# Optimization experiments

Measured on AMD Instinct MI355X. Metric: run time of the kernel, lower is better.

The kernel has to match this reference:

```python
import jax, jax.numpy as jnp
import numpy as np

B, H, W, K = 4, 512, 512, 8
BKG_DEPTH = 100.0  # sentinel depth for empty pixels, as in the torch module


def setup_inputs() -> dict:
    key = jax.random.key(0)
    k1, k2, k3 = jax.random.split(key, 3)
    pixel_colors = jax.random.uniform(k1, (B, H, W, K, 4), dtype=jnp.float32)
    zbuf = jax.random.normal(k2, (B, H, W, K), dtype=jnp.float32)  # <0 => invalid fragment
    pixel_labels = jax.random.randint(k3, (B, H, W, K), 0, K, dtype=jnp.int32)
    background_color = jnp.ones((3,), jnp.float32)
    return {
        "pixel_colors": pixel_colors,
        "zbuf": zbuf,
        "pixel_labels": pixel_labels,
        "background_color": background_color,
    }


def _composite(pixel_colors, zbuf, labels_f, background_color):
    """Back-to-front alpha-over compositing scan across the K layer axis."""
    Bq, Hq, Wq, Kd, _ = pixel_colors.shape
    # layer axis to front, reversed so scan runs k = K-1 .. 0 (back to front)
    cols = jnp.moveaxis(pixel_colors, 3, 0)[::-1]  # [K,B,H,W,4]
    deps = jnp.moveaxis(zbuf, 3, 0)[::-1]          # [K,B,H,W]
    labs = jnp.moveaxis(labels_f, 3, 0)[::-1]      # [K,B,H,W]

    rgb0 = jnp.broadcast_to(background_color.astype(pixel_colors.dtype), (Bq, Hq, Wq, 3)) + 0.0
    a0 = jnp.zeros((Bq, Hq, Wq), pixel_colors.dtype)
    d0 = jnp.full((Bq, Hq, Wq), BKG_DEPTH, pixel_colors.dtype)
    l0 = jnp.full((Bq, Hq, Wq), float(Kd), pixel_colors.dtype)

    def step(carry, x):
        rgb, a, d, lab = carry
        c, z, l = x
        alpha = c[..., 3]
        rgb = c[..., :3] * alpha[..., None] + rgb * (1.0 - alpha[..., None])
        a = jnp.maximum(alpha, a)
        d = jnp.where(z > 0, z * alpha + d * (1.0 - alpha), d)
        lab = jnp.where(jnp.isfinite(l), jnp.where(alpha > 0.5, l, lab), lab)
        return (rgb, a, d, lab), None

    (rgb, a, d, lab), _ = jax.lax.scan(step, (rgb0, a0, d0, l0), (cols, deps, labs))
    img = jnp.concatenate([rgb, a[..., None]], axis=-1)  # [B,H,W,4]
    return img, d, lab


def _human_images(pixel_colors, labels_int, background_color):
    """For each label n in [0,K): gather the first (front-most) fragment with that label."""
    Bq, Hq, Wq, Kd, C = pixel_colors.shape
    N = Kd
    hit = labels_int[..., None] == jnp.arange(N, dtype=labels_int.dtype)  # [B,H,W,K,N]
    hit = jnp.concatenate([hit, jnp.ones((Bq, Hq, Wq, 1, N), bool)], axis=3)  # void layer always hits
    first = jnp.argmax(hit, axis=3)  # [B,H,W,N], first k where label matches, else K
    pcv = jnp.concatenate(
        [pixel_colors, jnp.zeros((Bq, Hq, Wq, 1, C), pixel_colors.dtype)], axis=3
    )  # [B,H,W,K+1,4]
    gathered = jnp.take_along_axis(pcv, first[..., None], axis=3)  # [B,H,W,N,4]
    alpha = gathered[..., 3:4]
    rgb = gathered[..., :3] * alpha + background_color * (1.0 - alpha)
    return jnp.concatenate([rgb, alpha], axis=-1)  # [B,H,W,N,4]


def reference(pixel_colors, zbuf, pixel_labels, background_color):
    Kd = pixel_colors.shape[3]
    # labels as float with NaN marking invalid fragments (zbuf < 0), as in torch forward
    labels_f = jnp.where(zbuf < 0, jnp.nan, pixel_labels.astype(pixel_colors.dtype))
    composite_image, composite_depth, lab = _composite(pixel_colors, zbuf, labels_f, background_color)
    # labels as ints with -1 marking invalid, as in raster_each_labeled_human
    labels_int = jnp.where(zbuf < 0, -1, pixel_labels.astype(jnp.int32))
    human_images = _human_images(pixel_colors, labels_int, background_color)
    lab = jnp.where(lab > Kd - 0.5, -1.0, lab)
    composite_label = jnp.round(lab).astype(jnp.int32)
    return composite_image, composite_depth, composite_label, human_images
```

## Files before the change

### kernel.cpp

```cpp
#include <hip/hip_runtime.h>


#define BKG_DEPTH 100.0f
#define KD 8

__global__ __launch_bounds__(256) void alpha_comp_pixel(
    const float4* __restrict__ pc,
    const float4* __restrict__ zb4,
    const int4*   __restrict__ lb4,
    const float*  __restrict__ bg,
    float* __restrict__ out,
    int P)
{
    const int p = blockIdx.x * blockDim.x + threadIdx.x;
    if (p >= P) return;

    const float bg0 = bg[0], bg1 = bg[1], bg2 = bg[2];

    float4 c[KD];
    #pragma unroll
    for (int k = 0; k < KD; ++k) c[k] = pc[p * KD + k];

    const float4 zlo = zb4[p * 2 + 0];
    const float4 zhi = zb4[p * 2 + 1];
    const float z[KD] = {zlo.x, zlo.y, zlo.z, zlo.w, zhi.x, zhi.y, zhi.z, zhi.w};

    const int4 llo = lb4[p * 2 + 0];
    const int4 lhi = lb4[p * 2 + 1];
    const int l[KD] = {llo.x, llo.y, llo.z, llo.w, lhi.x, lhi.y, lhi.z, lhi.w};

    float T = 1.0f, r = 0.0f, g = 0.0f, b = 0.0f, am = 0.0f;
    #pragma unroll
    for (int k = 0; k < KD; ++k) {
        const float a = c[k].w;
        const float w = a * T;
        r = fmaf(c[k].x, w, r);
        g = fmaf(c[k].y, w, g);
        b = fmaf(c[k].z, w, b);
        am = fmaxf(am, a);
        T *= (1.0f - a);
    }
    r = fmaf(bg0, T, r);
    g = fmaf(bg1, T, g);
    b = fmaf(bg2, T, b);

    float T2 = 1.0f, d = 0.0f;
    #pragma unroll
    for (int k = 0; k < KD; ++k) {
        const float a2 = (z[k] > 0.0f) ? c[k].w : 0.0f;
        d = fmaf(z[k] * a2, T2, d);
        T2 *= (1.0f - a2);
    }
    d = fmaf(BKG_DEPTH, T2, d);

    float labv = -1.0f;
    #pragma unroll
    for (int k = KD - 1; k >= 0; --k) {
        const bool cond = (!(z[k] < 0.0f)) && (c[k].w > 0.5f);
        labv = cond ? (float)l[k] : labv;
    }

    ((float4*)out)[p] = make_float4(r, g, b, am);
    out[(size_t)4 * P + p] = d;
    out[(size_t)5 * P + p] = labv;

    float4* __restrict__ hout = (float4*)(out + (size_t)6 * P);
    #pragma unroll
    for (int n = 0; n < KD; ++n) {
        float gx = 0.0f, gy = 0.0f, gz = 0.0f, gw = 0.0f;
        #pragma unroll
        for (int k = KD - 1; k >= 0; --k) {
            const bool m = (!(z[k] < 0.0f)) && (l[k] == n);
            gx = m ? c[k].x : gx;
            gy = m ? c[k].y : gy;
            gz = m ? c[k].z : gz;
            gw = m ? c[k].w : gw;
        }
        const float ia = 1.0f - gw;
        hout[p * KD + n] = make_float4(fmaf(gx, gw, bg0 * ia),
                                       fmaf(gy, gw, bg1 * ia),
                                       fmaf(gz, gw, bg2 * ia),
                                       gw);
    }
}

extern "C" void kernel_launch(void* const* d_in, const int* in_sizes, int n_in,
                              void* d_out, int out_size, void* d_ws, size_t ws_size,
                              hipStream_t stream) {
    const float4* pc  = (const float4*)d_in[0];
    const float4* zb4 = (const float4*)d_in[1];
    const int4*   lb4 = (const int4*)d_in[2];
    const float*  bg  = (const float*)d_in[3];
    float* out = (float*)d_out;

    const int P = in_sizes[1] / KD;
    const int block = 256;
    const int grid = (P + block - 1) / block;
    alpha_comp_pixel<<<grid, block, 0, stream>>>(pc, zb4, lb4, bg, out, P);
}
```

Baseline: 326.4 us.

## Stage pixel colors and human-image outputs through swizzled LDS for coalesced access

```diff
diff --git a/kernel.cpp b/kernel.cpp
--- a/kernel.cpp
+++ b/kernel.cpp
@@ -3,8 +3,11 @@
 
 #define BKG_DEPTH 100.0f
 #define KD 8
+#define BLK 256
 
-__global__ __launch_bounds__(256) void alpha_comp_pixel(
+typedef float f32x4 __attribute__((ext_vector_type(4)));
+
+__global__ __launch_bounds__(256) void alpha_comp_lds(
     const float4* __restrict__ pc,
     const float4* __restrict__ zb4,
     const int4*   __restrict__ lb4,
@@ -12,22 +15,47 @@
     float* __restrict__ out,
     int P)
 {
-    const int p = blockIdx.x * blockDim.x + threadIdx.x;
-    if (p >= P) return;
+    __shared__ float4 cbuf[BLK * KD];
+
+    const int t    = threadIdx.x;
+    const int base = blockIdx.x * BLK;
+    const int p    = base + t;
+    const int pcl  = (p < P) ? p : (P - 1);
 
     const float bg0 = bg[0], bg1 = bg[1], bg2 = bg[2];
 
+    const float4 zlo = zb4[(size_t)pcl * 2 + 0];
+    const float4 zhi = zb4[(size_t)pcl * 2 + 1];
+    const int4   llo = lb4[(size_t)pcl * 2 + 0];
+    const int4   lhi = lb4[(size_t)pcl * 2 + 1];
+
+    {
+        const size_t fb = (size_t)base * KD;
+        const size_t fmax = (size_t)P * KD - 1;
+        float4 stg[8];
+        #pragma unroll
+        for (int i = 0; i < 8; ++i) {
+            size_t g = fb + i * BLK + t;
+            stg[i] = pc[g <= fmax ? g : fmax];
+        }
+        #pragma unroll
+        for (int i = 0; i < 8; ++i) {
+            const int g  = i * BLK + t;
+            const int pl = g >> 3;
+            const int k  = g & 7;
+            cbuf[pl * KD + (k ^ (pl & 7))] = stg[i];
+        }
+    }
+    __syncthreads();
+
     float4 c[KD];
     #pragma unroll
-    for (int k = 0; k < KD; ++k) c[k] = pc[p * KD + k];
+    for (int k = 0; k < KD; ++k)
+        c[k] = cbuf[t * KD + (k ^ (t & 7))];
+    __syncthreads();
 
-    const float4 zlo = zb4[p * 2 + 0];
-    const float4 zhi = zb4[p * 2 + 1];
     const float z[KD] = {zlo.x, zlo.y, zlo.z, zlo.w, zhi.x, zhi.y, zhi.z, zhi.w};
-
-    const int4 llo = lb4[p * 2 + 0];
-    const int4 lhi = lb4[p * 2 + 1];
-    const int l[KD] = {llo.x, llo.y, llo.z, llo.w, lhi.x, lhi.y, lhi.z, lhi.w};
+    const int   l[KD] = {llo.x, llo.y, llo.z, llo.w, lhi.x, lhi.y, lhi.z, lhi.w};
 
     float T = 1.0f, r = 0.0f, g = 0.0f, b = 0.0f, am = 0.0f;
     #pragma unroll
@@ -60,11 +88,12 @@
         labv = cond ? (float)l[k] : labv;
     }
 
-    ((float4*)out)[p] = make_float4(r, g, b, am);
-    out[(size_t)4 * P + p] = d;
-    out[(size_t)5 * P + p] = labv;
+    if (p < P) {
+        ((float4*)out)[p] = make_float4(r, g, b, am);
+        out[(size_t)4 * P + p] = d;
+        out[(size_t)5 * P + p] = labv;
+    }
 
-    float4* __restrict__ hout = (float4*)(out + (size_t)6 * P);
     #pragma unroll
     for (int n = 0; n < KD; ++n) {
         float gx = 0.0f, gy = 0.0f, gz = 0.0f, gw = 0.0f;
@@ -77,10 +106,28 @@
             gw = m ? c[k].w : gw;
         }
         const float ia = 1.0f - gw;
-        hout[p * KD + n] = make_float4(fmaf(gx, gw, bg0 * ia),
-                                       fmaf(gy, gw, bg1 * ia),
-                                       fmaf(gz, gw, bg2 * ia),
-                                       gw);
+        cbuf[t * KD + (n ^ (t & 7))] = make_float4(fmaf(gx, gw, bg0 * ia),
+                                                   fmaf(gy, gw, bg1 * ia),
+                                                   fmaf(gz, gw, bg2 * ia),
+                                                   gw);
+    }
+    __syncthreads();
+
+    {
+        f32x4* __restrict__ hout = (f32x4*)(out + (size_t)6 * P);
+        const size_t fb = (size_t)base * KD;
+        #pragma unroll
+        for (int i = 0; i < 8; ++i) {
+            const int g  = i * BLK + t;
+            const int pl = g >> 3;
+            const int n  = g & 7;
+            const float4 v = cbuf[pl * KD + (n ^ (pl & 7))];
+            const size_t go = fb + g;
+            if (go < (size_t)P * KD) {
+                f32x4 vv = {v.x, v.y, v.z, v.w};
+                __builtin_nontemporal_store(vv, &hout[go]);
+            }
+        }
     }
 }
 
@@ -94,7 +141,7 @@
     float* out = (float*)d_out;
 
     const int P = in_sizes[1] / KD;
-    const int block = 256;
+    const int block = BLK;
     const int grid = (P + block - 1) / block;
-    alpha_comp_pixel<<<grid, block, 0, stream>>>(pc, zb4, lb4, bg, out, P);
+    alpha_comp_lds<<<grid, block, 0, stream>>>(pc, zb4, lb4, bg, out, P);
 }
```

Result: faster. 308.2 us (-5.6%).

## Split each pixel across eight lanes with DPP scans and coalesced I/O

Applied to the files above, without the earlier changes.

```diff
diff --git a/kernel.cpp b/kernel.cpp
--- a/kernel.cpp
+++ b/kernel.cpp
@@ -4,97 +4,127 @@
 #define BKG_DEPTH 100.0f
 #define KD 8
 
-__global__ __launch_bounds__(256) void alpha_comp_pixel(
+typedef float f32x4 __attribute__((ext_vector_type(4)));
+
+#define QP_XOR1 0xB1
+#define QP_XOR2 0x4E
+#define ROW_SHL(n) (0x100 | (n))
+#define ROW_SHR(n) (0x110 | (n))
+
+template <int CTRL>
+__device__ __forceinline__ float dppf(float x) {
+    return __int_as_float(__builtin_amdgcn_update_dpp(
+        0, __float_as_int(x), CTRL, 0xF, 0xF, true));
+}
+template <int CTRL>
+__device__ __forceinline__ int dppi(int x) {
+    return __builtin_amdgcn_update_dpp(0, x, CTRL, 0xF, 0xF, true);
+}
+
+__global__ __launch_bounds__(256) void alpha_comp_dpp(
     const float4* __restrict__ pc,
-    const float4* __restrict__ zb4,
-    const int4*   __restrict__ lb4,
+    const float*  __restrict__ zb,
+    const int*    __restrict__ lb,
     const float*  __restrict__ bg,
     float* __restrict__ out,
     int P)
 {
-    const int p = blockIdx.x * blockDim.x + threadIdx.x;
-    if (p >= P) return;
+    const int tid = blockIdx.x * blockDim.x + threadIdx.x;
+    const int pix = tid >> 3;
+    const int kk  = tid & 7;
+    if (pix >= P) return;
 
     const float bg0 = bg[0], bg1 = bg[1], bg2 = bg[2];
 
-    float4 c[KD];
-    #pragma unroll
-    for (int k = 0; k < KD; ++k) c[k] = pc[p * KD + k];
+    const float4 c     = pc[tid];
+    const float  z     = zb[tid];
+    const int    lbl   = lb[tid];
+    const float  alpha = c.w;
+    const bool   valid = !(z < 0.0f);
 
-    const float4 zlo = zb4[p * 2 + 0];
-    const float4 zhi = zb4[p * 2 + 1];
-    const float z[KD] = {zlo.x, zlo.y, zlo.z, zlo.w, zhi.x, zhi.y, zhi.z, zhi.w};
+    float incl = 1.0f - alpha;
+    { const float u = dppf<ROW_SHR(1)>(incl); incl = (kk >= 1) ? incl * u : incl; }
+    { const float u = dppf<ROW_SHR(2)>(incl); incl = (kk >= 2) ? incl * u : incl; }
+    { const float u = dppf<ROW_SHR(4)>(incl); incl = (kk >= 4) ? incl * u : incl; }
+    float pre = dppf<ROW_SHR(1)>(incl); pre = (kk == 0) ? 1.0f : pre;
+    const float T = dppf<ROW_SHL(7)>(incl);
+    const float w = alpha * pre;
 
-    const int4 llo = lb4[p * 2 + 0];
-    const int4 lhi = lb4[p * 2 + 1];
-    const int l[KD] = {llo.x, llo.y, llo.z, llo.w, lhi.x, lhi.y, lhi.z, lhi.w};
+    float sr = c.x * w, sg = c.y * w, sb = c.z * w, am = alpha;
+    sr += dppf<QP_XOR1>(sr); sg += dppf<QP_XOR1>(sg); sb += dppf<QP_XOR1>(sb);
+    am = fmaxf(am, dppf<QP_XOR1>(am));
+    sr += dppf<QP_XOR2>(sr); sg += dppf<QP_XOR2>(sg); sb += dppf<QP_XOR2>(sb);
+    am = fmaxf(am, dppf<QP_XOR2>(am));
+    sr += dppf<ROW_SHL(4)>(sr); sg += dppf<ROW_SHL(4)>(sg); sb += dppf<ROW_SHL(4)>(sb);
+    am = fmaxf(am, dppf<ROW_SHL(4)>(am));
 
-    float T = 1.0f, r = 0.0f, g = 0.0f, b = 0.0f, am = 0.0f;
-    #pragma unroll
-    for (int k = 0; k < KD; ++k) {
-        const float a = c[k].w;
-        const float w = a * T;
-        r = fmaf(c[k].x, w, r);
-        g = fmaf(c[k].y, w, g);
-        b = fmaf(c[k].z, w, b);
-        am = fmaxf(am, a);
-        T *= (1.0f - a);
-    }
-    r = fmaf(bg0, T, r);
-    g = fmaf(bg1, T, g);
-    b = fmaf(bg2, T, b);
+    const float a2 = (z > 0.0f) ? alpha : 0.0f;
+    float incl2 = 1.0f - a2;
+    { const float u = dppf<ROW_SHR(1)>(incl2); incl2 = (kk >= 1) ? incl2 * u : incl2; }
+    { const float u = dppf<ROW_SHR(2)>(incl2); incl2 = (kk >= 2) ? incl2 * u : incl2; }
+    { const float u = dppf<ROW_SHR(4)>(incl2); incl2 = (kk >= 4) ? incl2 * u : incl2; }
+    float pre2 = dppf<ROW_SHR(1)>(incl2); pre2 = (kk == 0) ? 1.0f : pre2;
+    const float T2 = dppf<ROW_SHL(6)>(incl2);
+    float sd = z * (a2 * pre2);
+    sd += dppf<QP_XOR1>(sd);
+    sd += dppf<QP_XOR2>(sd);
+    sd += dppf<ROW_SHL(4)>(sd);
+    const float outD = fmaf(BKG_DEPTH, T2, sd);
 
-    float T2 = 1.0f, d = 0.0f;
-    #pragma unroll
-    for (int k = 0; k < KD; ++k) {
-        const float a2 = (z[k] > 0.0f) ? c[k].w : 0.0f;
-        d = fmaf(z[k] * a2, T2, d);
-        T2 *= (1.0f - a2);
-    }
-    d = fmaf(BKG_DEPTH, T2, d);
-
-    float labv = -1.0f;
-    #pragma unroll
-    for (int k = KD - 1; k >= 0; --k) {
-        const bool cond = (!(z[k] < 0.0f)) && (c[k].w > 0.5f);
-        labv = cond ? (float)l[k] : labv;
+    int pw = (valid ? lbl : 0xF) << (4 * kk);
+    pw |= dppi<QP_XOR1>(pw);
+    pw |= dppi<QP_XOR2>(pw);
+    {
+        const int lo = dppi<ROW_SHL(4)>(pw);
+        const int hi = dppi<ROW_SHR(4)>(pw);
+        pw |= (kk & 4) ? hi : lo;
     }
 
-    ((float4*)out)[p] = make_float4(r, g, b, am);
-    out[(size_t)4 * P + p] = d;
-    out[(size_t)5 * P + p] = labv;
+    const unsigned long long bal = __ballot(valid && (alpha > 0.5f));
+    const int lane = threadIdx.x & 63;
+    const unsigned grpByte = (unsigned)((bal >> (lane & ~7)) & 0xFFull);
+    const int jlab = grpByte ? (__ffs(grpByte) - 1) : 0;
+    const float labv = grpByte ? (float)((pw >> (4 * jlab)) & 0xF) : -1.0f;
 
-    float4* __restrict__ hout = (float4*)(out + (size_t)6 * P);
+    int jm = 8;
     #pragma unroll
-    for (int n = 0; n < KD; ++n) {
-        float gx = 0.0f, gy = 0.0f, gz = 0.0f, gw = 0.0f;
-        #pragma unroll
-        for (int k = KD - 1; k >= 0; --k) {
-            const bool m = (!(z[k] < 0.0f)) && (l[k] == n);
-            gx = m ? c[k].x : gx;
-            gy = m ? c[k].y : gy;
-            gz = m ? c[k].z : gz;
-            gw = m ? c[k].w : gw;
-        }
-        const float ia = 1.0f - gw;
-        hout[p * KD + n] = make_float4(fmaf(gx, gw, bg0 * ia),
-                                       fmaf(gy, gw, bg1 * ia),
-                                       fmaf(gz, gw, bg2 * ia),
-                                       gw);
+    for (int j = 7; j >= 0; --j)
+        jm = (((pw >> (4 * j)) & 0xF) == kk) ? j : jm;
+    const bool hit = (jm < 8);
+    const int src = hit ? jm : 0;
+    float gx = __shfl(c.x, src, 8);
+    float gy = __shfl(c.y, src, 8);
+    float gz = __shfl(c.z, src, 8);
+    float gw = __shfl(c.w, src, 8);
+    gx = hit ? gx : 0.0f;  gy = hit ? gy : 0.0f;
+    gz = hit ? gz : 0.0f;  gw = hit ? gw : 0.0f;
+    const float ia = 1.0f - gw;
+    const f32x4 hv = { fmaf(gx, gw, bg0 * ia),
+                       fmaf(gy, gw, bg1 * ia),
+                       fmaf(gz, gw, bg2 * ia),
+                       gw };
+
+    __builtin_nontemporal_store(hv, &((f32x4*)(out + (size_t)6 * P))[tid]);
+    if (kk == 0) {
+        const f32x4 img = { fmaf(bg0, T, sr), fmaf(bg1, T, sg), fmaf(bg2, T, sb), am };
+        __builtin_nontemporal_store(img, &((f32x4*)out)[pix]);
     }
+    if (kk == 1) __builtin_nontemporal_store(outD, &out[(size_t)4 * P + pix]);
+    if (kk == 2) __builtin_nontemporal_store(labv, &out[(size_t)5 * P + pix]);
 }
 
 extern "C" void kernel_launch(void* const* d_in, const int* in_sizes, int n_in,
                               void* d_out, int out_size, void* d_ws, size_t ws_size,
                               hipStream_t stream) {
-    const float4* pc  = (const float4*)d_in[0];
-    const float4* zb4 = (const float4*)d_in[1];
-    const int4*   lb4 = (const int4*)d_in[2];
-    const float*  bg  = (const float*)d_in[3];
+    const float4* pc = (const float4*)d_in[0];
+    const float*  zb = (const float*)d_in[1];
+    const int*    lb = (const int*)d_in[2];
+    const float*  bg = (const float*)d_in[3];
     float* out = (float*)d_out;
 
     const int P = in_sizes[1] / KD;
+    const int total = P * KD;
     const int block = 256;
-    const int grid = (P + block - 1) / block;
-    alpha_comp_pixel<<<grid, block, 0, stream>>>(pc, zb4, lb4, bg, out, P);
+    const int grid = (total + block - 1) / block;
+    alpha_comp_dpp<<<grid, block, 0, stream>>>(pc, zb, lb, bg, out, P);
 }
```

Measured after the change: 296.5 us. -9.1%, faster.
